# Kernel tuning notes

Measured on AMD Instinct MI355X. Metric: run time of the kernel, lower is better.

Reference implementation:

```python
import jax, jax.numpy as jnp
import numpy as np
import math

ORDER = 4
FREQ = 160


def _layernorm(x, g, b, eps=1e-5):
    m = jnp.mean(x, axis=-1, keepdims=True)
    v = jnp.mean((x - m) ** 2, axis=-1, keepdims=True)
    return (x - m) / jnp.sqrt(v + eps) * g + b


def setup_inputs() -> dict:
    key = jax.random.key(0)
    ks = jax.random.split(key, 9)
    b, t, k, f = 8, 1000, ORDER, FREQ
    return {
        "far_complex": jax.random.normal(ks[0], (b, 2, f, t), jnp.float32),
        "mix_complex": jax.random.normal(ks[1], (b, 2, f, t), jnp.float32),
        "k_conv_w": jax.random.normal(ks[2], (2 * k, 2), jnp.float32) * 0.3,   # Conv2d(2 -> 2k, 1x1)
        "k_conv_b": jax.random.normal(ks[3], (2 * k,), jnp.float32) * 0.01,
        "ql_w": jax.random.normal(ks[4], (f, f), jnp.float32) / math.sqrt(f),  # query_linear
        "ql_b": jnp.zeros((f,), jnp.float32),
        "qn_g": jnp.ones((f,), jnp.float32),   # query_norm gamma
        "qn_b": jnp.zeros((f,), jnp.float32),  # query_norm beta
        "kl_w": jax.random.normal(ks[5], (k, k), jnp.float32) / math.sqrt(k),  # key_linear
        "kl_b": jnp.zeros((k,), jnp.float32),
        "kn_g": jnp.ones((k,), jnp.float32),
        "kn_b": jnp.zeros((k,), jnp.float32),
        "q_vec": jax.random.normal(ks[6], (f,), jnp.float32) * 0.5,  # query_vector
        "k_vec": jax.random.normal(ks[7], (k,), jnp.float32) * 0.5,  # key_vector
        "v_vec": jax.random.normal(ks[8], (k,), jnp.float32) * 0.5,  # value_vector
    }


def reference(far_complex, mix_complex, k_conv_w, k_conv_b, ql_w, ql_b,
              qn_g, qn_b, kl_w, kl_b, kn_g, kn_b, q_vec, k_vec, v_vec):
    b, c, f, t = far_complex.shape
    k = k_vec.shape[0]

    # im2col-style unfold over time with left padding (k-1)
    padded = jnp.pad(far_complex, ((0, 0), (0, 0), (0, 0), (k - 1, 0)))
    idx = jnp.arange(t)[:, None] + jnp.arange(k)[None, :]          # [t, k]
    unf = padded[..., idx]                                          # [b,2,f,t,k]
    unf_save = unf[:, 0] + 1j * unf[:, 1]                           # [b,f,t,k] complex64
    # in-place conjugation of imag channel (as in torch code)
    unf = jnp.stack([unf[:, 0], -unf[:, 1]], axis=1)                # [b,2,f,t,k]

    # per-channel outer products (torch does real matmul per channel)
    XTX = jnp.einsum('bcfti,bcftj->bcftij', unf, unf)               # [b,2,f,t,k,k]
    XTY = (unf * mix_complex[..., None])[..., None]                 # [b,2,f,t,k,1]

    query = jnp.transpose(unf, (0, 1, 3, 4, 2))                     # [b,2,t,k,f]
    kc = jnp.einsum('oc,bcft->boft', k_conv_w, mix_complex) + k_conv_b[None, :, None, None]
    key = jnp.transpose(kc.reshape(b, 2, k, f, t), (0, 1, 4, 3, 2))  # [b,2,t,f,k]

    value = jnp.swapaxes(jnp.concatenate([XTX, XTY], axis=-1), -1, -2)  # [b,2,f,t,k+1,k]

    query = _layernorm(query @ ql_w.T + ql_b, qn_g, qn_b) * jax.nn.sigmoid(q_vec)
    key = _layernorm(key @ kl_w.T + kl_b, kn_g, kn_b) * jax.nn.sigmoid(k_vec)
    value = value * jax.nn.sigmoid(v_vec)

    weight = jax.nn.softmax(query @ (key / math.sqrt(k)), axis=-1)  # [b,2,t,k,k]
    out = value @ weight[:, :, None]                                # [b,2,f,t,k+1,k]
    outT = jnp.swapaxes(out, -1, -2)                                # [b,2,f,t,k,k+1]
    XTX_new = outT[..., :k]                                         # [b,2,f,t,k,k]
    XTY_new = outT[..., k:]                                         # [b,2,f,t,k,1]
    XTX_c = XTX_new[:, 0] + 1j * XTX_new[:, 1]                      # [b,f,t,k,k]
    XTY_c = XTY_new[:, 0] + 1j * XTY_new[:, 1]                      # [b,f,t,k,1]

    eps = 1e-8
    eye_r = jnp.eye(k, dtype=jnp.float32) + eps
    eye = (eye_r + 1j * eye_r).astype(XTX_c.dtype)

    inv_XTX = jnp.linalg.inv(XTX_c + eye)                           # [b,f,t,k,k]
    wiener = (inv_XTX @ XTY_c)[..., 0]                              # [b,f,t,k]

    res = jnp.sum(unf_save * wiener, axis=-1)                       # [b,f,t]
    return jnp.stack([res.real, res.imag], axis=1)                  # [b,2,f,t]
```

## Files before the change

kernel.cpp:

```cpp
#include <hip/hip_runtime.h>
#include <math.h>

#define NBC   16
#define NF    160
#define NT    1000

typedef __attribute__((ext_vector_type(8))) short short8;
typedef __attribute__((ext_vector_type(4))) float f32x4;

static __device__ __forceinline__ short f2bf(float x) {
    unsigned u = __builtin_bit_cast(unsigned, x);
    unsigned r = (u + 0x7fffu + ((u >> 16) & 1u)) >> 16;
    return (short)r;
}
static __device__ __forceinline__ float bf2f(short s) {
    unsigned u = ((unsigned)(unsigned short)s) << 16;
    return __builtin_bit_cast(float, u);
}

__global__ __launch_bounds__(1024, 4) void k13_fused(const float* __restrict__ far,
                                                     const float* __restrict__ mix,
                                                     const float* __restrict__ qlw,
                                                     const float* __restrict__ qlb,
                                                     const float* __restrict__ qng,
                                                     const float* __restrict__ qnb,
                                                     const float* __restrict__ qvec,
                                                     const float* __restrict__ kcw,
                                                     const float* __restrict__ kcb,
                                                     const float* __restrict__ klw,
                                                     const float* __restrict__ klb,
                                                     const float* __restrict__ kng,
                                                     const float* __restrict__ knb,
                                                     const float* __restrict__ kvec,
                                                     float* __restrict__ W) {
    __shared__ float pool[38720];
    __shared__ float lnM[80], lnI[80];
    float* Qlds = pool;
    float* Xs   = pool + 12960;
    short* Bhi  = (short*)(pool + 25920);
    short* Blo  = (short*)(pool + 32320);
    float* redS = Xs;
    float* redQ = Xs + 3280;
    float* sbuf = Xs;

    const int bc = blockIdx.x;
    const int t0 = blockIdx.y * 64;
    const int tid = threadIdx.x;
    const int w = __builtin_amdgcn_readfirstlane(tid >> 6);
    const int l = tid & 63;
    const int b = bc >> 1, c = bc & 1;
    const float sgn = c ? -1.f : 1.f;
    const float* Xb = far + (size_t)bc * NF * NT;

    const int row = l & 15;
    const int kb = l >> 4;

    short8 Ahi[5], Alo[5];
    if (w < 10) {
        #pragma unroll
        for (int fc = 0; fc < 5; ++fc) {
            const float* ap = qlw + (size_t)(16 * w + row) * NF + fc * 32 + kb * 8;
            float4 x0 = *(const float4*)(ap + 0);
            float4 x1 = *(const float4*)(ap + 4);
            float xv[8] = {x0.x, x0.y, x0.z, x0.w, x1.x, x1.y, x1.z, x1.w};
            short8 h, lo;
            #pragma unroll
            for (int j = 0; j < 8; ++j) {
                short hj = f2bf(xv[j]);
                h[j] = hj;
                lo[j] = f2bf(xv[j] - bf2f(hj));
            }
            Ahi[fc] = h; Alo[fc] = lo;
        }
    }

    #pragma unroll
    for (int i = 0; i < 13; ++i) {
        int o = tid + i * 1024;
        if (o < 12800) {
            int fi = o / 80, j = o - fi * 80;
            int tq = t0 - 3 + j;
            float v = (tq >= 0 && tq < NT) ? Xb[fi * NT + tq] * sgn : 0.f;
            Xs[fi * 81 + j] = v;
        }
    }
    __syncthreads();

    #pragma unroll
    for (int e = 0; e < 2; ++e) {
        int tk = tid + e * 1024;
        if (tk < 1600) {
            int g = tk >> 6;
            int sl = tk & 63;
            int tt = g / 5, fc = g - 5 * tt;
            int fi0 = fc * 32 + ((sl >> 4) << 3);
            int j0 = tt * 16 + (sl & 15);
            short8 h, lo;
            #pragma unroll
            for (int j = 0; j < 8; ++j) {
                float x = Xs[(fi0 + j) * 81 + j0];
                short hj = f2bf(x);
                h[j] = hj;
                lo[j] = f2bf(x - bf2f(hj));
            }
            *(short8*)&Bhi[tk * 8] = h;
            *(short8*)&Blo[tk * 8] = lo;
        }
    }
    __syncthreads();

    f32x4 acc0 = {0.f, 0.f, 0.f, 0.f}, acc1 = acc0, acc2 = acc0, acc3 = acc0, acc4 = acc0;
    float qlbv[4], gam[4], bet[4];
    if (w < 10) {
        #pragma unroll
        for (int fc = 0; fc < 5; ++fc) {
            #pragma unroll
            for (int tt = 0; tt < 5; ++tt) {
                short8 bh = *(const short8*)&Bhi[((tt * 5 + fc) * 64 + l) * 8];
                short8 bl = *(const short8*)&Blo[((tt * 5 + fc) * 64 + l) * 8];
                f32x4 a = (tt == 0) ? acc0 : (tt == 1) ? acc1 : (tt == 2) ? acc2 : (tt == 3) ? acc3 : acc4;
                a = __builtin_amdgcn_mfma_f32_16x16x32_bf16(Ahi[fc], bh, a, 0, 0, 0);
                a = __builtin_amdgcn_mfma_f32_16x16x32_bf16(Ahi[fc], bl, a, 0, 0, 0);
                a = __builtin_amdgcn_mfma_f32_16x16x32_bf16(Alo[fc], bh, a, 0, 0, 0);
                if (tt == 0) acc0 = a; else if (tt == 1) acc1 = a; else if (tt == 2) acc2 = a;
                else if (tt == 3) acc3 = a; else acc4 = a;
            }
        }
        #pragma unroll
        for (int r = 0; r < 4; ++r) {
            int fo = 16 * w + kb * 4 + r;
            qlbv[r] = qlb[fo];
            float sq = 1.f / (1.f + expf(-qvec[fo]));
            gam[r] = qng[fo] * sq;
            bet[r] = qnb[fo] * sq;
        }
        #pragma unroll
        for (int tt = 0; tt < 5; ++tt) {
            f32x4 a = (tt == 0) ? acc0 : (tt == 1) ? acc1 : (tt == 2) ? acc2 : (tt == 3) ? acc3 : acc4;
            float v0 = a[0] + qlbv[0], v1 = a[1] + qlbv[1];
            float v2 = a[2] + qlbv[2], v3 = a[3] + qlbv[3];
            int j = tt * 16 + row;
            redS[j * 41 + w * 4 + kb] = v0 + v1 + v2 + v3;
            redQ[j * 41 + w * 4 + kb] = v0 * v0 + v1 * v1 + v2 * v2 + v3 * v3;
        }
    }
    __syncthreads();

    if (tid < 80) {
        float s = 0.f, q = 0.f;
        #pragma unroll 8
        for (int j = 0; j < 40; ++j) {
            s += redS[tid * 41 + j];
            q += redQ[tid * 41 + j];
        }
        float mean = s * (1.f / NF);
        float var = q * (1.f / NF) - mean * mean;
        lnM[tid] = mean;
        lnI[tid] = 1.f / sqrtf(var + 1e-5f);
    }
    __syncthreads();

    if (w < 10) {
        #pragma unroll
        for (int tt = 0; tt < 5; ++tt) {
            f32x4 a = (tt == 0) ? acc0 : (tt == 1) ? acc1 : (tt == 2) ? acc2 : (tt == 3) ? acc3 : acc4;
            int j = tt * 16 + row;
            float mean = lnM[j], inv = lnI[j];
            #pragma unroll
            for (int r = 0; r < 4; ++r) {
                int fo = 16 * w + kb * 4 + r;
                float v = a[r] + qlbv[r];
                Qlds[fo * 81 + j] = (v - mean) * inv * gam[r] + bet[r];
            }
        }
    }
    __syncthreads();

    float kw0[4], kw1[4], kbv[4], klwm[16], klbv[4], kngv[4], knbv[4], sigk[4];
    #pragma unroll
    for (int j = 0; j < 4; ++j) {
        kw0[j] = kcw[(4 * c + j) * 2 + 0];
        kw1[j] = kcw[(4 * c + j) * 2 + 1];
        kbv[j] = kcb[4 * c + j];
        klbv[j] = klb[j];
        kngv[j] = kng[j];
        knbv[j] = knb[j];
        sigk[j] = 0.5f / (1.f + expf(-kvec[j]));
    }
    #pragma unroll
    for (int x = 0; x < 16; ++x) klwm[x] = klw[x];

    const int ts = l;
    const int t = t0 + ts;
    const bool valid = t < NT;

    float s[16];
    #pragma unroll
    for (int x = 0; x < 16; ++x) s[x] = 0.f;

    const float* mix0 = mix + (size_t)(b * 2) * NF * NT;
    const float* mix1 = mix0 + (size_t)NF * NT;
    const int f0 = w * 10;

    if (valid) {
        #pragma unroll
        for (int ff = 0; ff < 10; ++ff) {
            int f = f0 + ff;
            float m0 = mix0[(size_t)f * NT + t];
            float m1 = mix1[(size_t)f * NT + t];
            float kraw[4], klin[4];
            #pragma unroll
            for (int j = 0; j < 4; ++j)
                kraw[j] = fmaf(kw0[j], m0, fmaf(kw1[j], m1, kbv[j]));
            #pragma unroll
            for (int jo = 0; jo < 4; ++jo) {
                float a = klbv[jo];
                #pragma unroll
                for (int ji = 0; ji < 4; ++ji) a = fmaf(klwm[jo * 4 + ji], kraw[ji], a);
                klin[jo] = a;
            }
            float mn = 0.25f * (klin[0] + klin[1] + klin[2] + klin[3]);
            float d0 = klin[0] - mn, d1 = klin[1] - mn, d2 = klin[2] - mn, d3 = klin[3] - mn;
            float var = 0.25f * (d0 * d0 + d1 * d1 + d2 * d2 + d3 * d3);
            float inv = 1.f / sqrtf(var + 1e-5f);
            float kn[4];
            kn[0] = (d0 * inv * kngv[0] + knbv[0]) * sigk[0];
            kn[1] = (d1 * inv * kngv[1] + knbv[1]) * sigk[1];
            kn[2] = (d2 * inv * kngv[2] + knbv[2]) * sigk[2];
            kn[3] = (d3 * inv * kngv[3] + knbv[3]) * sigk[3];

            float q0 = Qlds[f * 81 + ts + 0];
            float q1 = Qlds[f * 81 + ts + 1];
            float q2 = Qlds[f * 81 + ts + 2];
            float q3 = Qlds[f * 81 + ts + 3];
            #pragma unroll
            for (int j = 0; j < 4; ++j) {
                s[0 * 4 + j] = fmaf(q0, kn[j], s[0 * 4 + j]);
                s[1 * 4 + j] = fmaf(q1, kn[j], s[1 * 4 + j]);
                s[2 * 4 + j] = fmaf(q2, kn[j], s[2 * 4 + j]);
                s[3 * 4 + j] = fmaf(q3, kn[j], s[3 * 4 + j]);
            }
        }
    }

    {
        float* dst = &sbuf[(w * 64 + l) * 17];
        #pragma unroll
        for (int q4 = 0; q4 < 4; ++q4) {
            float4 v = {s[q4 * 4 + 0], s[q4 * 4 + 1], s[q4 * 4 + 2], s[q4 * 4 + 3]};
            *(float4*)(dst + q4 * 4) = v;
        }
    }
    __syncthreads();

    if (tid < 256) {
        int q4 = tid >> 6;
        int ln = tid & 63;
        int tt = t0 + ln;
        if (tt < NT) {
            float4 a = *(const float4*)&sbuf[(0 * 64 + ln) * 17 + q4 * 4];
            #pragma unroll
            for (int ww = 1; ww < 16; ++ww) {
                float4 p = *(const float4*)&sbuf[(ww * 64 + ln) * 17 + q4 * 4];
                a.x += p.x; a.y += p.y; a.z += p.z; a.w += p.w;
            }
            float mx = fmaxf(fmaxf(a.x, a.y), fmaxf(a.z, a.w));
            float e0 = expf(a.x - mx), e1 = expf(a.y - mx);
            float e2 = expf(a.z - mx), e3 = expf(a.w - mx);
            float inv = 1.f / (e0 + e1 + e2 + e3);
            float4 v = {e0 * inv, e1 * inv, e2 * inv, e3 * inv};
            *(float4*)(W + ((size_t)bc * NT + tt) * 16 + q4 * 4) = v;
        }
    }
}

__device__ __forceinline__ void csolve4(float Ar[16], float Ai[16],
                                        float br[4], float bi[4],
                                        float wr[4], float wi[4]) {
    #pragma unroll
    for (int col = 0; col < 4; ++col) {
        #pragma unroll
        for (int r = col + 1; r < 4; ++r) {
            float cp = fabsf(Ar[col * 4 + col]) + fabsf(Ai[col * 4 + col]);
            float cr = fabsf(Ar[r * 4 + col]) + fabsf(Ai[r * 4 + col]);
            bool sw = cr > cp;
            #pragma unroll
            for (int m = col; m < 4; ++m) {
                float a0 = Ar[col * 4 + m], a1 = Ar[r * 4 + m];
                Ar[col * 4 + m] = sw ? a1 : a0;
                Ar[r * 4 + m]   = sw ? a0 : a1;
                float c0 = Ai[col * 4 + m], c1 = Ai[r * 4 + m];
                Ai[col * 4 + m] = sw ? c1 : c0;
                Ai[r * 4 + m]   = sw ? c0 : c1;
            }
            float b0 = br[col], b1 = br[r];
            br[col] = sw ? b1 : b0; br[r] = sw ? b0 : b1;
            float d0 = bi[col], d1 = bi[r];
            bi[col] = sw ? d1 : d0; bi[r] = sw ? d0 : d1;
        }
        float pr = Ar[col * 4 + col], pi = Ai[col * 4 + col];
        float den = 1.f / (pr * pr + pi * pi);
        #pragma unroll
        for (int r = col + 1; r < 4; ++r) {
            float nr = Ar[r * 4 + col], ni = Ai[r * 4 + col];
            float fr = (nr * pr + ni * pi) * den;
            float fi = (ni * pr - nr * pi) * den;
            #pragma unroll
            for (int m = col + 1; m < 4; ++m) {
                float tr = Ar[col * 4 + m], ti = Ai[col * 4 + m];
                Ar[r * 4 + m] -= fr * tr - fi * ti;
                Ai[r * 4 + m] -= fr * ti + fi * tr;
            }
            float tr = br[col], ti = bi[col];
            br[r] -= fr * tr - fi * ti;
            bi[r] -= fr * ti + fi * tr;
        }
    }
    #pragma unroll
    for (int col = 3; col >= 0; --col) {
        float sr = br[col], si = bi[col];
        #pragma unroll
        for (int m = col + 1; m < 4; ++m) {
            float tr = Ar[col * 4 + m], ti = Ai[col * 4 + m];
            sr -= tr * wr[m] - ti * wi[m];
            si -= tr * wi[m] + ti * wr[m];
        }
        float pr = Ar[col * 4 + col], pi = Ai[col * 4 + col];
        float den = 1.f / (pr * pr + pi * pi);
        wr[col] = (sr * pr + si * pi) * den;
        wi[col] = (si * pr - sr * pi) * den;
    }
}

__global__ __launch_bounds__(256) void k4_final(const float* __restrict__ far,
                                                const float* __restrict__ mix,
                                                const float* __restrict__ Wt,
                                                const float* __restrict__ vvec,
                                                float* __restrict__ out) {
    const int t = blockIdx.x * 256 + threadIdx.x;
    const int f = blockIdx.y;
    const int b = blockIdx.z;
    if (t >= NT) return;

    const float* fr  = far + (size_t)(b * 2 + 0) * NF * NT + (size_t)f * NT;
    const float* fim = far + (size_t)(b * 2 + 1) * NF * NT + (size_t)f * NT;
    float ur[4], ui[4];
    #pragma unroll
    for (int d = 0; d < 4; ++d) {
        int tp = t - 3 + d;
        bool ok = tp >= 0;
        ur[d] = ok ? fr[tp] : 0.f;
        ui[d] = ok ? fim[tp] : 0.f;
    }
    float m0 = mix[(size_t)(b * 2 + 0) * NF * NT + (size_t)f * NT + t];
    float m1 = mix[(size_t)(b * 2 + 1) * NF * NT + (size_t)f * NT + t];

    float sv[4];
    #pragma unroll
    for (int i = 0; i < 4; ++i) sv[i] = 1.f / (1.f + expf(-vvec[i]));

    const float* w0p = Wt + ((size_t)(b * 2 + 0) * NT + t) * 16;
    const float* w1p = Wt + ((size_t)(b * 2 + 1) * NT + t) * 16;

    float g0[4], g1[4];
    #pragma unroll
    for (int j = 0; j < 4; ++j) { g0[j] = 0.f; g1[j] = 0.f; }
    #pragma unroll
    for (int i = 0; i < 4; ++i) {
        float a0 = ur[i] * sv[i];
        float a1 = -ui[i] * sv[i];
        #pragma unroll
        for (int j = 0; j < 4; ++j) {
            g0[j] = fmaf(a0, w0p[i * 4 + j], g0[j]);
            g1[j] = fmaf(a1, w1p[i * 4 + j], g1[j]);
        }
    }

    float Ar[16], Ai[16], br[4], bi[4], wr[4], wi[4];
    #pragma unroll
    for (int j = 0; j < 4; ++j) {
        #pragma unroll
        for (int m = 0; m < 4; ++m) {
            float e = (j == m) ? (1.0f + 1e-8f) : 1e-8f;
            Ar[j * 4 + m] = fmaf(ur[m], g0[j], e);
            Ai[j * 4 + m] = fmaf(-ui[m], g1[j], e);
        }
        br[j] = m0 * g0[j];
        bi[j] = m1 * g1[j];
    }

    csolve4(Ar, Ai, br, bi, wr, wi);

    float resr = 0.f, resi = 0.f;
    #pragma unroll
    for (int d = 0; d < 4; ++d) {
        resr += ur[d] * wr[d] - ui[d] * wi[d];
        resi += ur[d] * wi[d] + ui[d] * wr[d];
    }
    out[(size_t)(b * 2 + 0) * NF * NT + (size_t)f * NT + t] = resr;
    out[(size_t)(b * 2 + 1) * NF * NT + (size_t)f * NT + t] = resi;
}

extern "C" void kernel_launch(void* const* d_in, const int* in_sizes, int n_in,
                              void* d_out, int out_size, void* d_ws, size_t ws_size,
                              hipStream_t stream) {
    const float* far  = (const float*)d_in[0];
    const float* mix  = (const float*)d_in[1];
    const float* kcw  = (const float*)d_in[2];
    const float* kcb  = (const float*)d_in[3];
    const float* qlw  = (const float*)d_in[4];
    const float* qlb  = (const float*)d_in[5];
    const float* qng  = (const float*)d_in[6];
    const float* qnb  = (const float*)d_in[7];
    const float* klw  = (const float*)d_in[8];
    const float* klb  = (const float*)d_in[9];
    const float* kng  = (const float*)d_in[10];
    const float* knb  = (const float*)d_in[11];
    const float* qvec = (const float*)d_in[12];
    const float* kvec = (const float*)d_in[13];
    const float* vvec = (const float*)d_in[14];

    float* W = (float*)d_ws;
    float* out = (float*)d_out;

    k13_fused<<<dim3(NBC, 16), 1024, 0, stream>>>(far, mix, qlw, qlb, qng, qnb, qvec,
                                                  kcw, kcb, klw, klb, kng, knb, kvec, W);
    k4_final<<<dim3(4, NF, 8), 256, 0, stream>>>(far, mix, W, vvec, out);
}
```

Measured before the change: 52.06 us.

## Shrink time tile to 32 with 640-thread blocks and direct bf16 split staging

The fused query/key kernel now works on 32-step time tiles instead of 64 and uses 640 threads (10 waves), so every wave does MFMA work and no waves sit idle. The grid grows from 16 to 32 tiles per batch-channel, which gives more blocks for the CUs to schedule, and shared memory drops to roughly half, allowing more resident blocks. Input values are converted to bf16 hi/lo and scattered straight into the MFMA B layout, which removes one staging pass and one barrier. In exchange, the halo and weight-conversion overhead per output grows, since the 3-column halo is now spread over 32 time steps rather than 64 and the qlw split is redone by twice as many blocks.

```diff
diff --git a/kernel.cpp b/kernel.cpp
--- a/kernel.cpp
+++ b/kernel.cpp
@@ -4,6 +4,9 @@
 #define NBC   16
 #define NF    160
 #define NT    1000
+#define TS    32
+#define JW    48
+#define QSTR  49
 
 typedef __attribute__((ext_vector_type(8))) short short8;
 typedef __attribute__((ext_vector_type(4))) float f32x4;
@@ -18,135 +21,112 @@
     return __builtin_bit_cast(float, u);
 }
 
-__global__ __launch_bounds__(1024, 4) void k13_fused(const float* __restrict__ far,
-                                                     const float* __restrict__ mix,
-                                                     const float* __restrict__ qlw,
-                                                     const float* __restrict__ qlb,
-                                                     const float* __restrict__ qng,
-                                                     const float* __restrict__ qnb,
-                                                     const float* __restrict__ qvec,
-                                                     const float* __restrict__ kcw,
-                                                     const float* __restrict__ kcb,
-                                                     const float* __restrict__ klw,
-                                                     const float* __restrict__ klb,
-                                                     const float* __restrict__ kng,
-                                                     const float* __restrict__ knb,
-                                                     const float* __restrict__ kvec,
-                                                     float* __restrict__ W) {
-    __shared__ float pool[38720];
-    __shared__ float lnM[80], lnI[80];
+__global__ __launch_bounds__(640, 5) void k13_fused(const float* __restrict__ far,
+                                                    const float* __restrict__ mix,
+                                                    const float* __restrict__ qlw,
+                                                    const float* __restrict__ qlb,
+                                                    const float* __restrict__ qng,
+                                                    const float* __restrict__ qnb,
+                                                    const float* __restrict__ qvec,
+                                                    const float* __restrict__ kcw,
+                                                    const float* __restrict__ kcb,
+                                                    const float* __restrict__ klw,
+                                                    const float* __restrict__ klb,
+                                                    const float* __restrict__ kng,
+                                                    const float* __restrict__ knb,
+                                                    const float* __restrict__ kvec,
+                                                    float* __restrict__ W) {
+    __shared__ float pool[18720];
+    __shared__ float lnM[48], lnI[48];
     float* Qlds = pool;
-    float* Xs   = pool + 12960;
-    short* Bhi  = (short*)(pool + 25920);
-    short* Blo  = (short*)(pool + 32320);
-    float* redS = Xs;
-    float* redQ = Xs + 3280;
-    float* sbuf = Xs;
+    float* regB = pool + 7840;
+    short* Bhi  = (short*)regB;
+    short* Blo  = Bhi + 7680;
+    float* redS = regB;
+    float* redQ = regB + 1968;
+    float* sbuf = regB;
 
     const int bc = blockIdx.x;
-    const int t0 = blockIdx.y * 64;
+    const int t0 = blockIdx.y * TS;
     const int tid = threadIdx.x;
     const int w = __builtin_amdgcn_readfirstlane(tid >> 6);
     const int l = tid & 63;
     const int b = bc >> 1, c = bc & 1;
     const float sgn = c ? -1.f : 1.f;
     const float* Xb = far + (size_t)bc * NF * NT;
-
     const int row = l & 15;
     const int kb = l >> 4;
 
     short8 Ahi[5], Alo[5];
-    if (w < 10) {
-        #pragma unroll
-        for (int fc = 0; fc < 5; ++fc) {
-            const float* ap = qlw + (size_t)(16 * w + row) * NF + fc * 32 + kb * 8;
-            float4 x0 = *(const float4*)(ap + 0);
-            float4 x1 = *(const float4*)(ap + 4);
-            float xv[8] = {x0.x, x0.y, x0.z, x0.w, x1.x, x1.y, x1.z, x1.w};
-            short8 h, lo;
-            #pragma unroll
-            for (int j = 0; j < 8; ++j) {
-                short hj = f2bf(xv[j]);
-                h[j] = hj;
-                lo[j] = f2bf(xv[j] - bf2f(hj));
-            }
-            Ahi[fc] = h; Alo[fc] = lo;
-        }
-    }
-
-    #pragma unroll
-    for (int i = 0; i < 13; ++i) {
-        int o = tid + i * 1024;
-        if (o < 12800) {
-            int fi = o / 80, j = o - fi * 80;
-            int tq = t0 - 3 + j;
-            float v = (tq >= 0 && tq < NT) ? Xb[fi * NT + tq] * sgn : 0.f;
-            Xs[fi * 81 + j] = v;
-        }
-    }
-    __syncthreads();
-
-    #pragma unroll
-    for (int e = 0; e < 2; ++e) {
-        int tk = tid + e * 1024;
-        if (tk < 1600) {
-            int g = tk >> 6;
-            int sl = tk & 63;
-            int tt = g / 5, fc = g - 5 * tt;
-            int fi0 = fc * 32 + ((sl >> 4) << 3);
-            int j0 = tt * 16 + (sl & 15);
-            short8 h, lo;
-            #pragma unroll
-            for (int j = 0; j < 8; ++j) {
-                float x = Xs[(fi0 + j) * 81 + j0];
-                short hj = f2bf(x);
-                h[j] = hj;
-                lo[j] = f2bf(x - bf2f(hj));
-            }
-            *(short8*)&Bhi[tk * 8] = h;
-            *(short8*)&Blo[tk * 8] = lo;
-        }
-    }
-    __syncthreads();
-
-    f32x4 acc0 = {0.f, 0.f, 0.f, 0.f}, acc1 = acc0, acc2 = acc0, acc3 = acc0, acc4 = acc0;
+    #pragma unroll
+    for (int fc = 0; fc < 5; ++fc) {
+        const float* ap = qlw + (size_t)(16 * w + row) * NF + fc * 32 + kb * 8;
+        float4 x0 = *(const float4*)(ap + 0);
+        float4 x1 = *(const float4*)(ap + 4);
+        float xv[8] = {x0.x, x0.y, x0.z, x0.w, x1.x, x1.y, x1.z, x1.w};
+        short8 h, lo;
+        #pragma unroll
+        for (int j = 0; j < 8; ++j) {
+            short hj = f2bf(xv[j]);
+            h[j] = hj;
+            lo[j] = f2bf(xv[j] - bf2f(hj));
+        }
+        Ahi[fc] = h; Alo[fc] = lo;
+    }
+
+    #pragma unroll
+    for (int i = 0; i < 12; ++i) {
+        int o = tid + i * 640;
+        int fi = o / JW, j = o - fi * JW;
+        int tq = t0 - 3 + j;
+        float v = (tq >= 0 && tq < NT) ? Xb[fi * NT + tq] * sgn : 0.f;
+        short hi = f2bf(v);
+        short lo = f2bf(v - bf2f(hi));
+        int slot = (j >> 4) * 5 + (fi >> 5);
+        int sl = (((fi & 31) >> 3) << 4) | (j & 15);
+        int idx = (slot * 64 + sl) * 8 + (fi & 7);
+        Bhi[idx] = hi;
+        Blo[idx] = lo;
+    }
+    __syncthreads();
+
+    f32x4 acc0 = {0.f, 0.f, 0.f, 0.f}, acc1 = acc0, acc2 = acc0;
+    #pragma unroll
+    for (int fc = 0; fc < 5; ++fc) {
+        #pragma unroll
+        for (int tt = 0; tt < 3; ++tt) {
+            short8 bh = *(const short8*)&Bhi[((tt * 5 + fc) * 64 + l) * 8];
+            short8 bl = *(const short8*)&Blo[((tt * 5 + fc) * 64 + l) * 8];
+            f32x4 a = (tt == 0) ? acc0 : (tt == 1) ? acc1 : acc2;
+            a = __builtin_amdgcn_mfma_f32_16x16x32_bf16(Ahi[fc], bh, a, 0, 0, 0);
+            a = __builtin_amdgcn_mfma_f32_16x16x32_bf16(Ahi[fc], bl, a, 0, 0, 0);
+            a = __builtin_amdgcn_mfma_f32_16x16x32_bf16(Alo[fc], bh, a, 0, 0, 0);
+            if (tt == 0) acc0 = a; else if (tt == 1) acc1 = a; else acc2 = a;
+        }
+    }
+    __syncthreads();
+
     float qlbv[4], gam[4], bet[4];
-    if (w < 10) {
-        #pragma unroll
-        for (int fc = 0; fc < 5; ++fc) {
-            #pragma unroll
-            for (int tt = 0; tt < 5; ++tt) {
-                short8 bh = *(const short8*)&Bhi[((tt * 5 + fc) * 64 + l) * 8];
-                short8 bl = *(const short8*)&Blo[((tt * 5 + fc) * 64 + l) * 8];
-                f32x4 a = (tt == 0) ? acc0 : (tt == 1) ? acc1 : (tt == 2) ? acc2 : (tt == 3) ? acc3 : acc4;
-                a = __builtin_amdgcn_mfma_f32_16x16x32_bf16(Ahi[fc], bh, a, 0, 0, 0);
-                a = __builtin_amdgcn_mfma_f32_16x16x32_bf16(Ahi[fc], bl, a, 0, 0, 0);
-                a = __builtin_amdgcn_mfma_f32_16x16x32_bf16(Alo[fc], bh, a, 0, 0, 0);
-                if (tt == 0) acc0 = a; else if (tt == 1) acc1 = a; else if (tt == 2) acc2 = a;
-                else if (tt == 3) acc3 = a; else acc4 = a;
-            }
-        }
-        #pragma unroll
-        for (int r = 0; r < 4; ++r) {
-            int fo = 16 * w + kb * 4 + r;
-            qlbv[r] = qlb[fo];
-            float sq = 1.f / (1.f + expf(-qvec[fo]));
-            gam[r] = qng[fo] * sq;
-            bet[r] = qnb[fo] * sq;
-        }
-        #pragma unroll
-        for (int tt = 0; tt < 5; ++tt) {
-            f32x4 a = (tt == 0) ? acc0 : (tt == 1) ? acc1 : (tt == 2) ? acc2 : (tt == 3) ? acc3 : acc4;
-            float v0 = a[0] + qlbv[0], v1 = a[1] + qlbv[1];
-            float v2 = a[2] + qlbv[2], v3 = a[3] + qlbv[3];
-            int j = tt * 16 + row;
-            redS[j * 41 + w * 4 + kb] = v0 + v1 + v2 + v3;
-            redQ[j * 41 + w * 4 + kb] = v0 * v0 + v1 * v1 + v2 * v2 + v3 * v3;
-        }
-    }
-    __syncthreads();
-
-    if (tid < 80) {
+    #pragma unroll
+    for (int r = 0; r < 4; ++r) {
+        int fo = 16 * w + kb * 4 + r;
+        qlbv[r] = qlb[fo];
+        float sq = 1.f / (1.f + expf(-qvec[fo]));
+        gam[r] = qng[fo] * sq;
+        bet[r] = qnb[fo] * sq;
+    }
+    #pragma unroll
+    for (int tt = 0; tt < 3; ++tt) {
+        f32x4 a = (tt == 0) ? acc0 : (tt == 1) ? acc1 : acc2;
+        float v0 = a[0] + qlbv[0], v1 = a[1] + qlbv[1];
+        float v2 = a[2] + qlbv[2], v3 = a[3] + qlbv[3];
+        int j = tt * 16 + row;
+        redS[j * 41 + w * 4 + kb] = v0 + v1 + v2 + v3;
+        redQ[j * 41 + w * 4 + kb] = v0 * v0 + v1 * v1 + v2 * v2 + v3 * v3;
+    }
+    __syncthreads();
+
+    if (tid < 48) {
         float s = 0.f, q = 0.f;
         #pragma unroll 8
         for (int j = 0; j < 40; ++j) {
@@ -160,18 +140,16 @@
     }
     __syncthreads();
 
-    if (w < 10) {
-        #pragma unroll
-        for (int tt = 0; tt < 5; ++tt) {
-            f32x4 a = (tt == 0) ? acc0 : (tt == 1) ? acc1 : (tt == 2) ? acc2 : (tt == 3) ? acc3 : acc4;
-            int j = tt * 16 + row;
-            float mean = lnM[j], inv = lnI[j];
-            #pragma unroll
-            for (int r = 0; r < 4; ++r) {
-                int fo = 16 * w + kb * 4 + r;
-                float v = a[r] + qlbv[r];
-                Qlds[fo * 81 + j] = (v - mean) * inv * gam[r] + bet[r];
-            }
+    #pragma unroll
+    for (int tt = 0; tt < 3; ++tt) {
+        f32x4 a = (tt == 0) ? acc0 : (tt == 1) ? acc1 : acc2;
+        int j = tt * 16 + row;
+        float mean = lnM[j], inv = lnI[j];
+        #pragma unroll
+        for (int r = 0; r < 4; ++r) {
+            int fo = 16 * w + kb * 4 + r;
+            float v = a[r] + qlbv[r];
+            Qlds[fo * QSTR + j] = (v - mean) * inv * gam[r] + bet[r];
         }
     }
     __syncthreads();
@@ -190,8 +168,9 @@
     #pragma unroll
     for (int x = 0; x < 16; ++x) klwm[x] = klw[x];
 
-    const int ts = l;
-    const int t = t0 + ts;
+    const int site = l & 31;
+    const int h = l >> 5;
+    const int t = t0 + site;
     const bool valid = t < NT;
 
     float s[16];
@@ -200,11 +179,11 @@
 
     const float* mix0 = mix + (size_t)(b * 2) * NF * NT;
     const float* mix1 = mix0 + (size_t)NF * NT;
-    const int f0 = w * 10;
+    const int f0 = w * 16 + h * 8;
 
     if (valid) {
         #pragma unroll
-        for (int ff = 0; ff < 10; ++ff) {
+        for (int ff = 0; ff < 8; ++ff) {
             int f = f0 + ff;
             float m0 = mix0[(size_t)f * NT + t];
             float m1 = mix1[(size_t)f * NT + t];
@@ -229,10 +208,10 @@
             kn[2] = (d2 * inv * kngv[2] + knbv[2]) * sigk[2];
             kn[3] = (d3 * inv * kngv[3] + knbv[3]) * sigk[3];
 
-            float q0 = Qlds[f * 81 + ts + 0];
-            float q1 = Qlds[f * 81 + ts + 1];
-            float q2 = Qlds[f * 81 + ts + 2];
-            float q3 = Qlds[f * 81 + ts + 3];
+            float q0 = Qlds[f * QSTR + site + 0];
+            float q1 = Qlds[f * QSTR + site + 1];
+            float q2 = Qlds[f * QSTR + site + 2];
+            float q3 = Qlds[f * QSTR + site + 3];
             #pragma unroll
             for (int j = 0; j < 4; ++j) {
                 s[0 * 4 + j] = fmaf(q0, kn[j], s[0 * 4 + j]);
@@ -244,7 +223,7 @@
     }
 
     {
-        float* dst = &sbuf[(w * 64 + l) * 17];
+        float* dst = &sbuf[((w * 2 + h) * 32 + site) * 17];
         #pragma unroll
         for (int q4 = 0; q4 < 4; ++q4) {
             float4 v = {s[q4 * 4 + 0], s[q4 * 4 + 1], s[q4 * 4 + 2], s[q4 * 4 + 3]};
@@ -253,15 +232,15 @@
     }
     __syncthreads();
 
-    if (tid < 256) {
-        int q4 = tid >> 6;
-        int ln = tid & 63;
+    if (tid < 128) {
+        int q4 = tid >> 5;
+        int ln = tid & 31;
         int tt = t0 + ln;
         if (tt < NT) {
-            float4 a = *(const float4*)&sbuf[(0 * 64 + ln) * 17 + q4 * 4];
-            #pragma unroll
-            for (int ww = 1; ww < 16; ++ww) {
-                float4 p = *(const float4*)&sbuf[(ww * 64 + ln) * 17 + q4 * 4];
+            float4 a = *(const float4*)&sbuf[(0 * 32 + ln) * 17 + q4 * 4];
+            #pragma unroll
+            for (int g = 1; g < 20; ++g) {
+                float4 p = *(const float4*)&sbuf[(g * 32 + ln) * 17 + q4 * 4];
                 a.x += p.x; a.y += p.y; a.z += p.z; a.w += p.w;
             }
             float mx = fmaxf(fmaxf(a.x, a.y), fmaxf(a.z, a.w));
@@ -423,7 +402,7 @@
     float* W = (float*)d_ws;
     float* out = (float*)d_out;
 
-    k13_fused<<<dim3(NBC, 16), 1024, 0, stream>>>(far, mix, qlw, qlb, qng, qnb, qvec,
-                                                  kcw, kcb, klw, klb, kng, knb, kvec, W);
+    k13_fused<<<dim3(NBC, (NT + TS - 1) / TS), 640, 0, stream>>>(
+        far, mix, qlw, qlb, qng, qnb, qvec, kcw, kcb, klw, klb, kng, knb, kvec, W);
     k4_final<<<dim3(4, NF, 8), 256, 0, stream>>>(far, mix, W, vvec, out);
 }
```

Measured after the change: 62.14 us. 19.4% more time.

## Stream far-input in frequency chunks with register prefetch, shrink LDS, fold key linear algebra

Applied to the files above, without the earlier changes.

The far-input tile is no longer staged fully in LDS and then converted. It is now loaded in 32-frequency chunks into registers, converted to hi/lo bf16 straight into a small B buffer, and the next chunk is prefetched while the MFMA runs on the current one. This cuts shared memory from about 155KB to about 70KB so more blocks can fit per CU, at the cost of extra barriers per chunk. Separately, the key conv plus key-linear plus mean subtraction is folded algebraically into per-block coefficients, which removes per-element matmul work in the score loop. A barrier is added before sbuf reuse because sbuf now aliases Qlds.

```diff
diff --git a/kernel.cpp b/kernel.cpp
--- a/kernel.cpp
+++ b/kernel.cpp
@@ -4,6 +4,8 @@
 #define NBC   16
 #define NF    160
 #define NT    1000
+#define TS    64
+#define QSTR  81
 
 typedef __attribute__((ext_vector_type(8))) short short8;
 typedef __attribute__((ext_vector_type(4))) float f32x4;
@@ -33,25 +35,23 @@
                                                      const float* __restrict__ knb,
                                                      const float* __restrict__ kvec,
                                                      float* __restrict__ W) {
-    __shared__ float pool[38720];
+    __shared__ float pool[17600];
     __shared__ float lnM[80], lnI[80];
     float* Qlds = pool;
-    float* Xs   = pool + 12960;
-    short* Bhi  = (short*)(pool + 25920);
-    short* Blo  = (short*)(pool + 32320);
-    float* redS = Xs;
-    float* redQ = Xs + 3280;
-    float* sbuf = Xs;
+    float* redS = pool;
+    float* redQ = pool + 3280;
+    short* Bhi  = (short*)(pool + 12960);
+    short* Blo  = (short*)(pool + 14240);
+    float* sbuf = pool;
 
     const int bc = blockIdx.x;
-    const int t0 = blockIdx.y * 64;
+    const int t0 = blockIdx.y * TS;
     const int tid = threadIdx.x;
     const int w = __builtin_amdgcn_readfirstlane(tid >> 6);
     const int l = tid & 63;
     const int b = bc >> 1, c = bc & 1;
     const float sgn = c ? -1.f : 1.f;
     const float* Xb = far + (size_t)bc * NF * NT;
-
     const int row = l & 15;
     const int kb = l >> 4;
 
@@ -74,50 +74,56 @@
         }
     }
 
-    #pragma unroll
-    for (int i = 0; i < 13; ++i) {
-        int o = tid + i * 1024;
-        if (o < 12800) {
-            int fi = o / 80, j = o - fi * 80;
+    f32x4 acc0 = {0.f, 0.f, 0.f, 0.f}, acc1 = acc0, acc2 = acc0, acc3 = acc0, acc4 = acc0;
+    float vcur0 = 0.f, vcur1 = 0.f, vcur2 = 0.f;
+
+    #pragma unroll
+    for (int i = 0; i < 3; ++i) {
+        int e = tid + i * 1024;
+        if (e < 2560) {
+            int fi_l = e / 80, j = e - fi_l * 80;
             int tq = t0 - 3 + j;
-            float v = (tq >= 0 && tq < NT) ? Xb[fi * NT + tq] * sgn : 0.f;
-            Xs[fi * 81 + j] = v;
-        }
-    }
-    __syncthreads();
-
-    #pragma unroll
-    for (int e = 0; e < 2; ++e) {
-        int tk = tid + e * 1024;
-        if (tk < 1600) {
-            int g = tk >> 6;
-            int sl = tk & 63;
-            int tt = g / 5, fc = g - 5 * tt;
-            int fi0 = fc * 32 + ((sl >> 4) << 3);
-            int j0 = tt * 16 + (sl & 15);
-            short8 h, lo;
-            #pragma unroll
-            for (int j = 0; j < 8; ++j) {
-                float x = Xs[(fi0 + j) * 81 + j0];
-                short hj = f2bf(x);
-                h[j] = hj;
-                lo[j] = f2bf(x - bf2f(hj));
-            }
-            *(short8*)&Bhi[tk * 8] = h;
-            *(short8*)&Blo[tk * 8] = lo;
-        }
-    }
-    __syncthreads();
-
-    f32x4 acc0 = {0.f, 0.f, 0.f, 0.f}, acc1 = acc0, acc2 = acc0, acc3 = acc0, acc4 = acc0;
-    float qlbv[4], gam[4], bet[4];
-    if (w < 10) {
-        #pragma unroll
-        for (int fc = 0; fc < 5; ++fc) {
+            float v = (tq >= 0 && tq < NT) ? Xb[(size_t)fi_l * NT + tq] * sgn : 0.f;
+            if (i == 0) vcur0 = v; else if (i == 1) vcur1 = v; else vcur2 = v;
+        }
+    }
+
+    #pragma unroll
+    for (int fc = 0; fc < 5; ++fc) {
+        #pragma unroll
+        for (int i = 0; i < 3; ++i) {
+            int e = tid + i * 1024;
+            if (e < 2560) {
+                int fi_l = e / 80, j = e - fi_l * 80;
+                int tt = j >> 4;
+                int sl = ((fi_l >> 3) << 4) | (j & 15);
+                int idx = (tt * 64 + sl) * 8 + (fi_l & 7);
+                float v = (i == 0) ? vcur0 : (i == 1) ? vcur1 : vcur2;
+                short hi = f2bf(v);
+                Bhi[idx] = hi;
+                Blo[idx] = f2bf(v - bf2f(hi));
+            }
+        }
+        float vn0 = 0.f, vn1 = 0.f, vn2 = 0.f;
+        if (fc < 4) {
+            #pragma unroll
+            for (int i = 0; i < 3; ++i) {
+                int e = tid + i * 1024;
+                if (e < 2560) {
+                    int fi_l = e / 80, j = e - fi_l * 80;
+                    int tq = t0 - 3 + j;
+                    int fi = (fc + 1) * 32 + fi_l;
+                    float v = (tq >= 0 && tq < NT) ? Xb[(size_t)fi * NT + tq] * sgn : 0.f;
+                    if (i == 0) vn0 = v; else if (i == 1) vn1 = v; else vn2 = v;
+                }
+            }
+        }
+        __syncthreads();
+        if (w < 10) {
             #pragma unroll
             for (int tt = 0; tt < 5; ++tt) {
-                short8 bh = *(const short8*)&Bhi[((tt * 5 + fc) * 64 + l) * 8];
-                short8 bl = *(const short8*)&Blo[((tt * 5 + fc) * 64 + l) * 8];
+                short8 bh = *(const short8*)&Bhi[(tt * 64 + l) * 8];
+                short8 bl = *(const short8*)&Blo[(tt * 64 + l) * 8];
                 f32x4 a = (tt == 0) ? acc0 : (tt == 1) ? acc1 : (tt == 2) ? acc2 : (tt == 3) ? acc3 : acc4;
                 a = __builtin_amdgcn_mfma_f32_16x16x32_bf16(Ahi[fc], bh, a, 0, 0, 0);
                 a = __builtin_amdgcn_mfma_f32_16x16x32_bf16(Ahi[fc], bl, a, 0, 0, 0);
@@ -126,6 +132,12 @@
                 else if (tt == 3) acc3 = a; else acc4 = a;
             }
         }
+        __syncthreads();
+        vcur0 = vn0; vcur1 = vn1; vcur2 = vn2;
+    }
+
+    float qlbv[4], gam[4], bet[4];
+    if (w < 10) {
         #pragma unroll
         for (int r = 0; r < 4; ++r) {
             int fo = 16 * w + kb * 4 + r;
@@ -170,28 +182,42 @@
             for (int r = 0; r < 4; ++r) {
                 int fo = 16 * w + kb * 4 + r;
                 float v = a[r] + qlbv[r];
-                Qlds[fo * 81 + j] = (v - mean) * inv * gam[r] + bet[r];
+                Qlds[fo * QSTR + j] = (v - mean) * inv * gam[r] + bet[r];
             }
         }
     }
     __syncthreads();
 
-    float kw0[4], kw1[4], kbv[4], klwm[16], klbv[4], kngv[4], knbv[4], sigk[4];
-    #pragma unroll
-    for (int j = 0; j < 4; ++j) {
-        kw0[j] = kcw[(4 * c + j) * 2 + 0];
-        kw1[j] = kcw[(4 * c + j) * 2 + 1];
-        kbv[j] = kcb[4 * c + j];
-        klbv[j] = klb[j];
-        kngv[j] = kng[j];
-        knbv[j] = knb[j];
-        sigk[j] = 0.5f / (1.f + expf(-kvec[j]));
-    }
-    #pragma unroll
-    for (int x = 0; x < 16; ++x) klwm[x] = klw[x];
-
-    const int ts = l;
-    const int t = t0 + ts;
+    float alpha[4], beta4[4], gamm[4], G[4], H[4];
+    {
+        float M0[4], M1[4], B4[4];
+        #pragma unroll
+        for (int jo = 0; jo < 4; ++jo) {
+            float m0 = 0.f, m1 = 0.f, bb = klb[jo];
+            #pragma unroll
+            for (int ji = 0; ji < 4; ++ji) {
+                float kl = klw[jo * 4 + ji];
+                m0 = fmaf(kl, kcw[(4 * c + ji) * 2 + 0], m0);
+                m1 = fmaf(kl, kcw[(4 * c + ji) * 2 + 1], m1);
+                bb = fmaf(kl, kcb[4 * c + ji], bb);
+            }
+            M0[jo] = m0; M1[jo] = m1; B4[jo] = bb;
+        }
+        float am = 0.25f * (M0[0] + M0[1] + M0[2] + M0[3]);
+        float bm = 0.25f * (M1[0] + M1[1] + M1[2] + M1[3]);
+        float cm = 0.25f * (B4[0] + B4[1] + B4[2] + B4[3]);
+        #pragma unroll
+        for (int jo = 0; jo < 4; ++jo) {
+            alpha[jo] = M0[jo] - am;
+            beta4[jo] = M1[jo] - bm;
+            gamm[jo]  = B4[jo] - cm;
+            float sk = 0.5f / (1.f + expf(-kvec[jo]));
+            G[jo] = kng[jo] * sk;
+            H[jo] = knb[jo] * sk;
+        }
+    }
+
+    const int t = t0 + l;
     const bool valid = t < NT;
 
     float s[16];
@@ -208,31 +234,22 @@
             int f = f0 + ff;
             float m0 = mix0[(size_t)f * NT + t];
             float m1 = mix1[(size_t)f * NT + t];
-            float kraw[4], klin[4];
-            #pragma unroll
-            for (int j = 0; j < 4; ++j)
-                kraw[j] = fmaf(kw0[j], m0, fmaf(kw1[j], m1, kbv[j]));
-            #pragma unroll
-            for (int jo = 0; jo < 4; ++jo) {
-                float a = klbv[jo];
-                #pragma unroll
-                for (int ji = 0; ji < 4; ++ji) a = fmaf(klwm[jo * 4 + ji], kraw[ji], a);
-                klin[jo] = a;
-            }
-            float mn = 0.25f * (klin[0] + klin[1] + klin[2] + klin[3]);
-            float d0 = klin[0] - mn, d1 = klin[1] - mn, d2 = klin[2] - mn, d3 = klin[3] - mn;
+            float d0 = fmaf(alpha[0], m0, fmaf(beta4[0], m1, gamm[0]));
+            float d1 = fmaf(alpha[1], m0, fmaf(beta4[1], m1, gamm[1]));
+            float d2 = fmaf(alpha[2], m0, fmaf(beta4[2], m1, gamm[2]));
+            float d3 = fmaf(alpha[3], m0, fmaf(beta4[3], m1, gamm[3]));
             float var = 0.25f * (d0 * d0 + d1 * d1 + d2 * d2 + d3 * d3);
             float inv = 1.f / sqrtf(var + 1e-5f);
             float kn[4];
-            kn[0] = (d0 * inv * kngv[0] + knbv[0]) * sigk[0];
-            kn[1] = (d1 * inv * kngv[1] + knbv[1]) * sigk[1];
-            kn[2] = (d2 * inv * kngv[2] + knbv[2]) * sigk[2];
-            kn[3] = (d3 * inv * kngv[3] + knbv[3]) * sigk[3];
-
-            float q0 = Qlds[f * 81 + ts + 0];
-            float q1 = Qlds[f * 81 + ts + 1];
-            float q2 = Qlds[f * 81 + ts + 2];
-            float q3 = Qlds[f * 81 + ts + 3];
+            kn[0] = fmaf(d0 * inv, G[0], H[0]);
+            kn[1] = fmaf(d1 * inv, G[1], H[1]);
+            kn[2] = fmaf(d2 * inv, G[2], H[2]);
+            kn[3] = fmaf(d3 * inv, G[3], H[3]);
+
+            float q0 = Qlds[f * QSTR + l + 0];
+            float q1 = Qlds[f * QSTR + l + 1];
+            float q2 = Qlds[f * QSTR + l + 2];
+            float q3 = Qlds[f * QSTR + l + 3];
             #pragma unroll
             for (int j = 0; j < 4; ++j) {
                 s[0 * 4 + j] = fmaf(q0, kn[j], s[0 * 4 + j]);
@@ -242,6 +259,7 @@
             }
         }
     }
+    __syncthreads();
 
     {
         float* dst = &sbuf[(w * 64 + l) * 17];
@@ -423,7 +441,7 @@
     float* W = (float*)d_ws;
     float* out = (float*)d_out;
 
-    k13_fused<<<dim3(NBC, 16), 1024, 0, stream>>>(far, mix, qlw, qlb, qng, qnb, qvec,
-                                                  kcw, kcb, klw, klb, kng, knb, kvec, W);
+    k13_fused<<<dim3(NBC, (NT + TS - 1) / TS), 1024, 0, stream>>>(
+        far, mix, qlw, qlb, qng, qnb, qvec, kcw, kcb, klw, klb, kng, knb, kvec, W);
     k4_final<<<dim3(4, NF, 8), 256, 0, stream>>>(far, mix, W, vvec, out);
 }
```

After: 52.48 us. About the same (+0.8%).
